# Performance work log

Hardware: AMD Instinct MI355X
Metric: run time of the kernel (lower is better)

The kernel has to match this reference:

```python
import jax, jax.numpy as jnp
import numpy as np
from jax import lax

EPS = 1e-5
C = 232          # inp == oup
BF = C // 2      # branch_features
GROUPS = 2


def bn(x, g, b, m, v):
    # inference batchnorm over channel axis 1 of NCHW
    scale = g / jnp.sqrt(v + EPS)
    return x * scale[None, :, None, None] + (b - m * scale)[None, :, None, None]


def prelu(x, a):
    return jnp.where(x >= 0, x, a.reshape(()) * x)


def conv1x1(x, w):
    # x: [B,C,H,W], w: [O,C]
    return jnp.einsum('bchw,oc->bohw', x, w)


def dwconv3x3(x, w):
    # depthwise 3x3, stride 1, pad 1; w: [C,1,3,3]
    return lax.conv_general_dilated(
        x, w, window_strides=(1, 1), padding=((1, 1), (1, 1)),
        feature_group_count=x.shape[1],
        dimension_numbers=('NCHW', 'OIHW', 'NCHW'))


def setup_inputs() -> dict:
    key = jax.random.key(0)
    ks = jax.random.split(key, 12)
    B, H, W = 64, 56, 56
    inp = {
        'x': jax.random.normal(ks[0], (B, C, H, W), jnp.float32),
        'w2': jax.random.normal(ks[1], (BF, BF), jnp.float32) * 0.1,
        'bn1_g': jax.random.uniform(ks[2], (BF,), jnp.float32, 0.5, 1.5),
        'bn1_b': jax.random.normal(ks[3], (BF,), jnp.float32) * 0.1,
        'bn1_m': jax.random.normal(ks[4], (BF,), jnp.float32) * 0.1,
        'bn1_v': jax.random.uniform(ks[5], (BF,), jnp.float32, 0.5, 1.5),
        'alpha1': jnp.full((1,), 0.25, jnp.float32),
        'wdw': jax.random.normal(ks[6], (BF, 1, 3, 3), jnp.float32) * 0.1,
        'bn2_g': jax.random.uniform(ks[7], (BF,), jnp.float32, 0.5, 1.5),
        'bn2_b': jax.random.normal(ks[8], (BF,), jnp.float32) * 0.1,
        'bn2_m': jax.random.normal(ks[9], (BF,), jnp.float32) * 0.1,
        'bn2_v': jax.random.uniform(ks[10], (BF,), jnp.float32, 0.5, 1.5),
        'w3': jax.random.normal(ks[11], (BF, BF), jnp.float32) * 0.1,
        'bn3_g': jax.random.uniform(jax.random.fold_in(key, 101), (BF,), jnp.float32, 0.5, 1.5),
        'bn3_b': jax.random.normal(jax.random.fold_in(key, 102), (BF,)) * 0.1,
        'bn3_m': jax.random.normal(jax.random.fold_in(key, 103), (BF,)) * 0.1,
        'bn3_v': jax.random.uniform(jax.random.fold_in(key, 104), (BF,), jnp.float32, 0.5, 1.5),
        'alpha2': jnp.full((1,), 0.25, jnp.float32),
    }
    return inp


def reference(x, w2, bn1_g, bn1_b, bn1_m, bn1_v, alpha1, wdw,
              bn2_g, bn2_b, bn2_m, bn2_v, w3, bn3_g, bn3_b, bn3_m, bn3_v, alpha2):
    # stride == 1 path: split channels in half
    x1, x2 = x[:, :BF], x[:, BF:]
    # branch2: 1x1 conv -> BN -> PReLU -> dw3x3 -> BN -> 1x1 conv -> BN -> PReLU
    h = prelu(bn(conv1x1(x2, w2), bn1_g, bn1_b, bn1_m, bn1_v), alpha1)
    h = bn(dwconv3x3(h, wdw), bn2_g, bn2_b, bn2_m, bn2_v)
    h = prelu(bn(conv1x1(h, w3), bn3_g, bn3_b, bn3_m, bn3_v), alpha2)
    out = jnp.concatenate([x1, h], axis=1)
    # channel shuffle (groups=2): out channel k reads input channel (k%2)*cpg + k//2
    cpg = C // GROUPS
    idx = (jnp.arange(C) % GROUPS) * cpg + jnp.arange(C) // GROUPS
    return out[:, idx]
```

## Files before the change

### kernel.cpp

```cpp
#include <hip/hip_runtime.h>
#include <hip/hip_bf16.h>


#define BATCH 64
#define CTOT  232
#define BFC   116
#define HW    3136
#define WD    56
#define CH2   120
#define EPSV  1e-5f

typedef unsigned short u16;
typedef __attribute__((ext_vector_type(8))) short short8;
typedef __attribute__((ext_vector_type(4))) float float4v;

#define WS_W2P   0
#define WS_W3P   32768
#define WS_WDWT  65536
#define WS_B1P   69888
#define WS_B3P   70400
#define WS_XT    131072

__device__ __forceinline__ u16 f2bf(float f) {
    union { float f; unsigned u; } v; v.f = f;
    unsigned r = v.u + 0x7FFF + ((v.u >> 16) & 1);
    return (u16)(r >> 16);
}
__device__ __forceinline__ float bf2f(u16 u) {
    union { unsigned u; float f; } v; v.u = ((unsigned)u) << 16;
    return v.f;
}

__global__ __launch_bounds__(256) void prep(
    const float* __restrict__ w2, const float* __restrict__ g1, const float* __restrict__ b1,
    const float* __restrict__ m1, const float* __restrict__ v1,
    const float* __restrict__ wdw,
    const float* __restrict__ g2, const float* __restrict__ b2,
    const float* __restrict__ m2, const float* __restrict__ v2,
    const float* __restrict__ w3, const float* __restrict__ g3, const float* __restrict__ b3,
    const float* __restrict__ m3, const float* __restrict__ v3,
    char* __restrict__ ws) {
    u16* w2p = (u16*)(ws + WS_W2P);
    u16* w3p = (u16*)(ws + WS_W3P);
    float* wdwt = (float*)(ws + WS_WDWT);
    float* b1p = (float*)(ws + WS_B1P);
    float* b3p = (float*)(ws + WS_B3P);
    int tid = threadIdx.x;
    int bx = blockIdx.x;
    if (bx < 8) {
        int o = bx * 16 + (tid >> 4);
        int cs = (tid & 15) * 8;
        float sc = (o < BFC) ? g1[o] * rsqrtf(v1[o] + EPSV) : 0.f;
        short8 v;
        for (int j = 0; j < 8; j++) {
            int c = cs + j;
            float val = (o < BFC && c < BFC) ? sc * w2[o * BFC + c] : 0.f;
            ((u16*)&v)[j] = f2bf(val);
        }
        *(short8*)&w2p[o * 128 + cs] = v;
    } else if (bx < 16) {
        int o = (bx - 8) * 16 + (tid >> 4);
        int cs = (tid & 15) * 8;
        float sc = (o < BFC) ? g3[o] * rsqrtf(v3[o] + EPSV) : 0.f;
        short8 v;
        for (int j = 0; j < 8; j++) {
            int c = cs + j;
            float val = 0.f;
            if (o < BFC && c < BFC) {
                float sc2 = g2[c] * rsqrtf(v2[c] + EPSV);
                val = sc * sc2 * w3[o * BFC + c];
            }
            ((u16*)&v)[j] = f2bf(val);
        }
        *(short8*)&w3p[o * 128 + cs] = v;
    } else {
        if (tid < CH2)
            for (int tap = 0; tap < 9; tap++)
                wdwt[tap * CH2 + tid] = (tid < BFC) ? wdw[tid * 9 + tap] : 0.f;
        if (tid < 128) {
            float b1v = 0.f, b3v = 0.f;
            if (tid < BFC) {
                float sc1 = g1[tid] * rsqrtf(v1[tid] + EPSV);
                b1v = b1[tid] - m1[tid] * sc1;
                float sc3 = g3[tid] * rsqrtf(v3[tid] + EPSV);
                float s = 0.f;
                for (int c = 0; c < BFC; c++) {
                    float sc2 = g2[c] * rsqrtf(v2[c] + EPSV);
                    float sh2 = b2[c] - m2[c] * sc2;
                    s += w3[tid * BFC + c] * sh2;
                }
                b3v = (b3[tid] - m3[tid] * sc3) + sc3 * s;
            }
            b1p[tid] = b1v;
            b3p[tid] = b3v;
        }
    }
}

__global__ __launch_bounds__(256) void t0(const float* __restrict__ x, char* __restrict__ ws) {
    __shared__ u16 lt[64 * CH2];
    int tid = threadIdx.x;
    int b = blockIdx.y;
    int px0 = blockIdx.x * 64;
    const float* x2 = x + ((size_t)b * CTOT + BFC) * HW;
    u16* xt = (u16*)(ws + WS_XT);
    lt[(tid >> 2) * CH2 + BFC + (tid & 3)] = 0;
    for (int u = tid; u < 58 * 16; u += 256) {
        int c2 = u >> 4, i = u & 15;
        int c = c2 * 2;
        int p = px0 + i * 4;
        float4v va = *(const float4v*)&x2[(size_t)c * HW + p];
        float4v vb = *(const float4v*)&x2[(size_t)(c + 1) * HW + p];
        #pragma unroll
        for (int j = 0; j < 4; j++) {
            unsigned pair = (unsigned)f2bf(va[j]) | ((unsigned)f2bf(vb[j]) << 16);
            *(unsigned*)&lt[(i * 4 + j) * CH2 + c] = pair;
        }
    }
    __syncthreads();
    for (int u = tid; u < 64 * 15; u += 256) {
        int px = u / 15, oct = u % 15;
        short8 v = *(const short8*)&lt[px * CH2 + oct * 8];
        *(short8*)&xt[((size_t)b * HW + px0 + px) * CH2 + oct * 8] = v;
    }
}

__device__ __forceinline__ void dw_compute(const u16* h1s, const float* __restrict__ wdwt,
                                           int u, short8 hrow[4]) {
    int oct = u % 15;
    int pq = u / 15;
    int rr = pq / 14;
    int col0 = (pq % 14) * 4;
    float acc[4][8];
    #pragma unroll
    for (int i = 0; i < 4; i++)
        #pragma unroll
        for (int j = 0; j < 8; j++) acc[i][j] = 0.f;
    #pragma unroll
    for (int dy = 0; dy < 3; dy++) {
        int lr = rr + dy;
        float f[6][8];
        #pragma unroll
        for (int k = 0; k < 6; k++) {
            int ci = col0 - 1 + k;
            if (ci >= 0 && ci < WD) {
                short8 v = *(const short8*)&h1s[(lr * WD + ci) * CH2 + oct * 8];
                #pragma unroll
                for (int j = 0; j < 8; j++) f[k][j] = bf2f(((const u16*)&v)[j]);
            } else {
                #pragma unroll
                for (int j = 0; j < 8; j++) f[k][j] = 0.f;
            }
        }
        #pragma unroll
        for (int dx = 0; dx < 3; dx++) {
            const float* wt = &wdwt[(dy * 3 + dx) * CH2 + oct * 8];
            float4v w0 = *(const float4v*)&wt[0];
            float4v w1 = *(const float4v*)&wt[4];
            float w8[8] = {w0[0], w0[1], w0[2], w0[3], w1[0], w1[1], w1[2], w1[3]};
            #pragma unroll
            for (int i = 0; i < 4; i++)
                #pragma unroll
                for (int j = 0; j < 8; j++)
                    acc[i][j] += f[i + dx][j] * w8[j];
        }
    }
    #pragma unroll
    for (int i = 0; i < 4; i++) {
        short8 ov;
        #pragma unroll
        for (int j = 0; j < 8; j++) ((u16*)&ov)[j] = f2bf(acc[i][j]);
        hrow[i] = ov;
    }
}

__global__ __launch_bounds__(256, 3) void k1(const float* __restrict__ x,
        const float* __restrict__ al1, const float* __restrict__ al2,
        char* __restrict__ ws, float* __restrict__ out) {
    __shared__ u16 h1s[224 * CH2];
    const u16* w2p = (const u16*)(ws + WS_W2P);
    const u16* w3p = (const u16*)(ws + WS_W3P);
    const float* wdwt = (const float*)(ws + WS_WDWT);
    const float* b1p = (const float*)(ws + WS_B1P);
    const float* b3p = (const float*)(ws + WS_B3P);
    const u16* xt = (const u16*)(ws + WS_XT);

    int tid = threadIdx.x;
    int lane = tid & 63;
    int w = tid >> 6;
    int l15 = lane & 15, kq = lane >> 4;
    int b = blockIdx.y;
    int r0 = blockIdx.x * 2;
    int p_in0 = r0 * WD - WD;
    int p_out0 = r0 * WD;

    const u16* xtb = xt + (size_t)b * HW * CH2;
    float a1 = al1[0];
    short8 z8 = {0, 0, 0, 0, 0, 0, 0, 0};

    int mh = w >> 1, nh = w & 1;
    {
        short8 bfr[4][4];
        float biasv[4];
        for (int ni = 0; ni < 4; ni++) {
            int o = (nh * 4 + ni) * 16 + l15;
            #pragma unroll
            for (int kt = 0; kt < 4; kt++)
                bfr[ni][kt] = *(const short8*)&w2p[o * 128 + kt * 32 + kq * 8];
            biasv[ni] = b1p[o];
        }
        #pragma unroll
        for (int mi = 0; mi < 7; mi++) {
            int mt = mh * 7 + mi;
            int p = p_in0 + mt * 16 + l15;
            bool pv = (p >= 0) && (p < HW);
            const u16* arow = xtb + (size_t)p * CH2;
            short8 afr[4];
            #pragma unroll
            for (int kt = 0; kt < 4; kt++) {
                short8 av = z8;
                if (pv && !(kt == 3 && kq == 3)) av = *(const short8*)&arow[kt * 32 + kq * 8];
                afr[kt] = av;
            }
            for (int ni = 0; ni < 4; ni++) {
                float4v acc = {0.f, 0.f, 0.f, 0.f};
                #pragma unroll
                for (int kt = 0; kt < 4; kt++)
                    acc = __builtin_amdgcn_mfma_f32_16x16x32_bf16(afr[kt], bfr[ni][kt], acc, 0, 0, 0);
                int o = (nh * 4 + ni) * 16 + l15;
                if (o < CH2) {
                    int plb = mt * 16 + kq * 4;
                    #pragma unroll
                    for (int r = 0; r < 4; r++) {
                        int pl = plb + r;
                        int pim = p_in0 + pl;
                        float y = acc[r] + biasv[ni];
                        y = y >= 0.f ? y : a1 * y;
                        h1s[pl * CH2 + o] = (pim >= 0 && pim < HW) ? f2bf(y) : (u16)0;
                    }
                }
            }
        }
    }
    __syncthreads();

    short8 hA[4], hB[4];
    int uA = tid, uB = tid + 256;
    bool hasB = uB < 420;
    dw_compute(h1s, wdwt, uA, hA);
    if (hasB) dw_compute(h1s, wdwt, uB, hB);
    __syncthreads();

    {
        int oct = uA % 15, pq = uA / 15;
        int pl = (pq / 14) * WD + (pq % 14) * 4;
        #pragma unroll
        for (int i = 0; i < 4; i++)
            *(short8*)&h1s[(pl + i) * CH2 + oct * 8] = hA[i];
    }
    if (hasB) {
        int oct = uB % 15, pq = uB / 15;
        int pl = (pq / 14) * WD + (pq % 14) * 4;
        #pragma unroll
        for (int i = 0; i < 4; i++)
            *(short8*)&h1s[(pl + i) * CH2 + oct * 8] = hB[i];
    }
    __syncthreads();

    {
        float a2 = al2[0];
        short8 cfr[4][4];
        float bias3v[4];
        for (int ni = 0; ni < 4; ni++) {
            int o = (nh * 4 + ni) * 16 + l15;
            #pragma unroll
            for (int kt = 0; kt < 4; kt++)
                cfr[ni][kt] = *(const short8*)&w3p[o * 128 + kt * 32 + kq * 8];
            bias3v[ni] = b3p[o];
        }
        #pragma unroll
        for (int mi = 0; mi < 4; mi++) {
            int mt = mh * 4 + mi;
            if (mt < 7) {
                int pl = mt * 16 + l15;
                const u16* arow = &h1s[pl * CH2];
                short8 afr[4];
                #pragma unroll
                for (int kt = 0; kt < 4; kt++) {
                    short8 av = z8;
                    if (!(kt == 3 && kq == 3)) av = *(const short8*)&arow[kt * 32 + kq * 8];
                    afr[kt] = av;
                }
                for (int ni = 0; ni < 4; ni++) {
                    float4v acc = {0.f, 0.f, 0.f, 0.f};
                    #pragma unroll
                    for (int kt = 0; kt < 4; kt++)
                        acc = __builtin_amdgcn_mfma_f32_16x16x32_bf16(afr[kt], cfr[ni][kt], acc, 0, 0, 0);
                    int o = (nh * 4 + ni) * 16 + l15;
                    int pq = mt * 16 + kq * 4;
                    if (o < BFC) {
                        float4v ov;
                        #pragma unroll
                        for (int r = 0; r < 4; r++) {
                            float y = acc[r] + bias3v[ni];
                            ov[r] = y >= 0.f ? y : a2 * y;
                        }
                        *(float4v*)&out[((size_t)b * CTOT + 2 * o + 1) * HW + p_out0 + pq] = ov;
                    }
                }
            }
        }
    }

    {
        const float* x1 = x + (size_t)b * CTOT * HW;
        for (int u = tid; u < BFC * 28; u += 256) {
            int c = u / 28, i = u % 28;
            float4v v = *(const float4v*)&x1[(size_t)c * HW + p_out0 + i * 4];
            *(float4v*)&out[((size_t)b * CTOT + 2 * c) * HW + p_out0 + i * 4] = v;
        }
    }
}

extern "C" void kernel_launch(void* const* d_in, const int* in_sizes, int n_in,
                              void* d_out, int out_size, void* d_ws, size_t ws_size,
                              hipStream_t stream) {
    const float* x   = (const float*)d_in[0];
    const float* w2  = (const float*)d_in[1];
    const float* g1  = (const float*)d_in[2];
    const float* b1  = (const float*)d_in[3];
    const float* m1  = (const float*)d_in[4];
    const float* v1  = (const float*)d_in[5];
    const float* al1 = (const float*)d_in[6];
    const float* wdw = (const float*)d_in[7];
    const float* g2  = (const float*)d_in[8];
    const float* b2  = (const float*)d_in[9];
    const float* m2  = (const float*)d_in[10];
    const float* v2  = (const float*)d_in[11];
    const float* w3  = (const float*)d_in[12];
    const float* g3  = (const float*)d_in[13];
    const float* b3  = (const float*)d_in[14];
    const float* m3  = (const float*)d_in[15];
    const float* v3  = (const float*)d_in[16];
    const float* al2 = (const float*)d_in[17];
    float* out = (float*)d_out;
    char* ws = (char*)d_ws;

    hipLaunchKernelGGL(prep, dim3(17), dim3(256), 0, stream,
                       w2, g1, b1, m1, v1, wdw, g2, b2, m2, v2, w3, g3, b3, m3, v3, ws);
    hipLaunchKernelGGL(t0, dim3(HW / 64, BATCH), dim3(256), 0, stream, x, ws);
    hipLaunchKernelGGL(k1, dim3(28, BATCH), dim3(256), 0, stream, x, al1, al2, ws, out);
}
```

Before: 621.8 us.

## Fuse input transpose into main kernel, staging x tile in LDS

Removes the separate t0 kernel that converted x2 to a bf16 pixel-major workspace. Each k1 block now loads its fp32 input rows (with a one-row halo) straight from x, converts them to bf16 and stores them in LDS. The first 1x1 GEMM reads A from LDS, and its output overwrites the same buffer in place, which needs a __syncthreads per m-tile. The grid becomes 1D with a swizzled block-to-(batch, row) mapping meant to spread work across XCDs. This avoids writing and re-reading an intermediate tensor, but halo rows are loaded twice and the extra barriers add serialization.

```diff
diff --git a/kernel.cpp b/kernel.cpp
--- a/kernel.cpp
+++ b/kernel.cpp
@@ -19,7 +19,6 @@
 #define WS_WDWT  65536
 #define WS_B1P   69888
 #define WS_B3P   70400
-#define WS_XT    131072
 
 __device__ __forceinline__ u16 f2bf(float f) {
     union { float f; unsigned u; } v; v.f = f;
@@ -97,35 +96,7 @@
     }
 }
 
-__global__ __launch_bounds__(256) void t0(const float* __restrict__ x, char* __restrict__ ws) {
-    __shared__ u16 lt[64 * CH2];
-    int tid = threadIdx.x;
-    int b = blockIdx.y;
-    int px0 = blockIdx.x * 64;
-    const float* x2 = x + ((size_t)b * CTOT + BFC) * HW;
-    u16* xt = (u16*)(ws + WS_XT);
-    lt[(tid >> 2) * CH2 + BFC + (tid & 3)] = 0;
-    for (int u = tid; u < 58 * 16; u += 256) {
-        int c2 = u >> 4, i = u & 15;
-        int c = c2 * 2;
-        int p = px0 + i * 4;
-        float4v va = *(const float4v*)&x2[(size_t)c * HW + p];
-        float4v vb = *(const float4v*)&x2[(size_t)(c + 1) * HW + p];
-        #pragma unroll
-        for (int j = 0; j < 4; j++) {
-            unsigned pair = (unsigned)f2bf(va[j]) | ((unsigned)f2bf(vb[j]) << 16);
-            *(unsigned*)&lt[(i * 4 + j) * CH2 + c] = pair;
-        }
-    }
-    __syncthreads();
-    for (int u = tid; u < 64 * 15; u += 256) {
-        int px = u / 15, oct = u % 15;
-        short8 v = *(const short8*)&lt[px * CH2 + oct * 8];
-        *(short8*)&xt[((size_t)b * HW + px0 + px) * CH2 + oct * 8] = v;
-    }
-}
-
-__device__ __forceinline__ void dw_compute(const u16* h1s, const float* __restrict__ wdwt,
+__device__ __forceinline__ void dw_compute(const u16* xs, const float* __restrict__ wdwt,
                                            int u, short8 hrow[4]) {
     int oct = u % 15;
     int pq = u / 15;
@@ -144,7 +115,7 @@
         for (int k = 0; k < 6; k++) {
             int ci = col0 - 1 + k;
             if (ci >= 0 && ci < WD) {
-                short8 v = *(const short8*)&h1s[(lr * WD + ci) * CH2 + oct * 8];
+                short8 v = *(const short8*)&xs[(lr * WD + ci) * CH2 + oct * 8];
                 #pragma unroll
                 for (int j = 0; j < 8; j++) f[k][j] = bf2f(((const u16*)&v)[j]);
             } else {
@@ -176,67 +147,97 @@
 
 __global__ __launch_bounds__(256, 3) void k1(const float* __restrict__ x,
         const float* __restrict__ al1, const float* __restrict__ al2,
-        char* __restrict__ ws, float* __restrict__ out) {
-    __shared__ u16 h1s[224 * CH2];
+        const char* __restrict__ ws, float* __restrict__ out) {
+    __shared__ u16 xs[224 * CH2];
     const u16* w2p = (const u16*)(ws + WS_W2P);
     const u16* w3p = (const u16*)(ws + WS_W3P);
     const float* wdwt = (const float*)(ws + WS_WDWT);
     const float* b1p = (const float*)(ws + WS_B1P);
     const float* b3p = (const float*)(ws + WS_B3P);
-    const u16* xt = (const u16*)(ws + WS_XT);
 
     int tid = threadIdx.x;
     int lane = tid & 63;
     int w = tid >> 6;
     int l15 = lane & 15, kq = lane >> 4;
-    int b = blockIdx.y;
-    int r0 = blockIdx.x * 2;
+
+    int L = blockIdx.x;
+    int sw = (L & 7) * 224 + (L >> 3);
+    int b = sw / 28;
+    int s = sw - b * 28;
+    int r0 = s * 2;
     int p_in0 = r0 * WD - WD;
     int p_out0 = r0 * WD;
 
-    const u16* xtb = xt + (size_t)b * HW * CH2;
+    const float* x2 = x + ((size_t)b * CTOT + BFC) * HW;
     float a1 = al1[0];
+    float a2 = al2[0];
     short8 z8 = {0, 0, 0, 0, 0, 0, 0, 0};
 
-    int mh = w >> 1, nh = w & 1;
+    #pragma unroll 4
+    for (int it = 0; it < 14; it++) {
+        int u = it * 256 + tid;
+        int c2 = (u >> 3) & 63;
+        if (c2 < 60) {
+            int q = (u >> 9) * 8 + (u & 7);
+            int p = p_in0 + q * 4;
+            unsigned pr[4] = {0u, 0u, 0u, 0u};
+            if (c2 < 58 && p >= 0 && p < HW) {
+                int c = 2 * c2;
+                float4v va = *(const float4v*)&x2[(size_t)c * HW + p];
+                float4v vb = *(const float4v*)&x2[(size_t)(c + 1) * HW + p];
+                #pragma unroll
+                for (int j = 0; j < 4; j++)
+                    pr[j] = (unsigned)f2bf(va[j]) | ((unsigned)f2bf(vb[j]) << 16);
+            }
+            int px = q * 4;
+            #pragma unroll
+            for (int j = 0; j < 4; j++)
+                *(unsigned*)&xs[(px + j) * CH2 + 2 * c2] = pr[j];
+        }
+    }
+    __syncthreads();
+
     {
-        short8 bfr[4][4];
-        float biasv[4];
-        for (int ni = 0; ni < 4; ni++) {
-            int o = (nh * 4 + ni) * 16 + l15;
+        short8 bfr[2][4];
+        float biasv[2];
+        for (int ni = 0; ni < 2; ni++) {
+            int o = (2 * w + ni) * 16 + l15;
             #pragma unroll
             for (int kt = 0; kt < 4; kt++)
                 bfr[ni][kt] = *(const short8*)&w2p[o * 128 + kt * 32 + kq * 8];
             biasv[ni] = b1p[o];
         }
-        #pragma unroll
-        for (int mi = 0; mi < 7; mi++) {
-            int mt = mh * 7 + mi;
-            int p = p_in0 + mt * 16 + l15;
-            bool pv = (p >= 0) && (p < HW);
-            const u16* arow = xtb + (size_t)p * CH2;
+        for (int mt = 0; mt < 14; mt++) {
+            int pl = mt * 16 + l15;
+            const u16* arow = &xs[pl * CH2];
             short8 afr[4];
             #pragma unroll
             for (int kt = 0; kt < 4; kt++) {
                 short8 av = z8;
-                if (pv && !(kt == 3 && kq == 3)) av = *(const short8*)&arow[kt * 32 + kq * 8];
+                if (!(kt == 3 && kq == 3)) av = *(const short8*)&arow[kt * 32 + kq * 8];
                 afr[kt] = av;
             }
-            for (int ni = 0; ni < 4; ni++) {
-                float4v acc = {0.f, 0.f, 0.f, 0.f};
+            float4v acc[2];
+            #pragma unroll
+            for (int ni = 0; ni < 2; ni++) {
+                acc[ni] = (float4v){0.f, 0.f, 0.f, 0.f};
                 #pragma unroll
                 for (int kt = 0; kt < 4; kt++)
-                    acc = __builtin_amdgcn_mfma_f32_16x16x32_bf16(afr[kt], bfr[ni][kt], acc, 0, 0, 0);
-                int o = (nh * 4 + ni) * 16 + l15;
+                    acc[ni] = __builtin_amdgcn_mfma_f32_16x16x32_bf16(afr[kt], bfr[ni][kt], acc[ni], 0, 0, 0);
+            }
+            __syncthreads();
+            #pragma unroll
+            for (int ni = 0; ni < 2; ni++) {
+                int o = (2 * w + ni) * 16 + l15;
                 if (o < CH2) {
                     int plb = mt * 16 + kq * 4;
                     #pragma unroll
                     for (int r = 0; r < 4; r++) {
-                        int pl = plb + r;
-                        int pim = p_in0 + pl;
-                        float y = acc[r] + biasv[ni];
+                        int pl2 = plb + r;
+                        int pim = p_in0 + pl2;
+                        float y = acc[ni][r] + biasv[ni];
                         y = y >= 0.f ? y : a1 * y;
-                        h1s[pl * CH2 + o] = (pim >= 0 && pim < HW) ? f2bf(y) : (u16)0;
+                        xs[pl2 * CH2 + o] = (pim >= 0 && pim < HW) ? f2bf(y) : (u16)0;
                     }
                 }
             }
@@ -247,28 +248,27 @@
     short8 hA[4], hB[4];
     int uA = tid, uB = tid + 256;
     bool hasB = uB < 420;
-    dw_compute(h1s, wdwt, uA, hA);
-    if (hasB) dw_compute(h1s, wdwt, uB, hB);
+    dw_compute(xs, wdwt, uA, hA);
+    if (hasB) dw_compute(xs, wdwt, uB, hB);
     __syncthreads();
-
     {
         int oct = uA % 15, pq = uA / 15;
         int pl = (pq / 14) * WD + (pq % 14) * 4;
         #pragma unroll
         for (int i = 0; i < 4; i++)
-            *(short8*)&h1s[(pl + i) * CH2 + oct * 8] = hA[i];
+            *(short8*)&xs[(pl + i) * CH2 + oct * 8] = hA[i];
     }
     if (hasB) {
         int oct = uB % 15, pq = uB / 15;
         int pl = (pq / 14) * WD + (pq % 14) * 4;
         #pragma unroll
         for (int i = 0; i < 4; i++)
-            *(short8*)&h1s[(pl + i) * CH2 + oct * 8] = hB[i];
+            *(short8*)&xs[(pl + i) * CH2 + oct * 8] = hB[i];
     }
     __syncthreads();
 
     {
-        float a2 = al2[0];
+        int mh = w >> 1, nh = w & 1;
         short8 cfr[4][4];
         float bias3v[4];
         for (int ni = 0; ni < 4; ni++) {
@@ -283,7 +283,7 @@
             int mt = mh * 4 + mi;
             if (mt < 7) {
                 int pl = mt * 16 + l15;
-                const u16* arow = &h1s[pl * CH2];
+                const u16* arow = &xs[pl * CH2];
                 short8 afr[4];
                 #pragma unroll
                 for (int kt = 0; kt < 4; kt++) {
@@ -348,6 +348,5 @@
 
     hipLaunchKernelGGL(prep, dim3(17), dim3(256), 0, stream,
                        w2, g1, b1, m1, v1, wdw, g2, b2, m2, v2, w3, g3, b3, m3, v3, ws);
-    hipLaunchKernelGGL(t0, dim3(HW / 64, BATCH), dim3(256), 0, stream, x, ws);
-    hipLaunchKernelGGL(k1, dim3(28, BATCH), dim3(256), 0, stream, x, al1, al2, ws, out);
-}
+    hipLaunchKernelGGL(k1, dim3(28 * BATCH), dim3(256), 0, stream, x, al1, al2, ws, out);
+}
```

Result: faster. 575.7 us (-7.4%).
